# Optimization experiments

Measured on AMD Instinct MI355X. Metric: run time of the kernel, lower is better.

Reference implementation:

```python
import jax, jax.numpy as jnp
import numpy as np

ALPHA = 0.005
SCALE = 0.001
DELTA = 0.1
MAX_ITER = 50
EARLY = True


def setup_inputs() -> dict:
    key = jax.random.key(0)
    k1, k2, k3 = jax.random.split(key, 3)
    B, S, M, N = 32, 8, 512, 512
    x = jax.random.uniform(k1, (B, S, N), dtype=jnp.float32)
    A = jax.random.normal(k2, (B, S, M, N), dtype=jnp.float32) * 0.1
    b = jax.random.uniform(k3, (B, S, M), dtype=jnp.float32)
    return {"x": x, "A": A, "b": b}


def reference(x, A, b):
    # x: [B,S,N] primal iterate; A: [B,S,M,N] constraint matrices; b: [B,S,M]
    B, S = b.shape[0], b.shape[1]
    active0 = jnp.ones((B, S), dtype=bool)

    def body(carry, _):
        x_, active, stopped = carry
        # torch loop runs an iteration only while any(active) and not early-stopped
        run = jnp.any(active) & (~stopped)
        # Ax - b, clamped at 0 -> per-constraint violation
        Ax = jnp.einsum('bsn,bsmn->bsm', x_, A)          # [B,S,M]
        viol = jnp.clip(Ax - b, 0.0)
        new_active = jnp.sum(viol, axis=-1) >= DELTA      # ~(total < delta)
        stop_early = jnp.asarray(EARLY) & (~jnp.any(new_active))
        g = jnp.einsum('bsm,bsmn->bsn', viol, A)          # penalty gradient [B,S,N]
        lr = ALPHA / (1.0 + SCALE * g)
        x_upd = jnp.where(new_active[..., None], x_ - lr * g, x_)
        x_upd = jnp.clip(x_upd, 0.0)                      # clamp applied even to inactive rows
        # early stop happens BEFORE the update/clamp in the torch code
        x_new = jnp.where(stop_early, x_, x_upd)
        x_out = jnp.where(run, x_new, x_)
        active_out = jnp.where(run, new_active, active)
        stopped_out = stopped | (run & stop_early)
        return (x_out, active_out, stopped_out), None

    # torch: break when count > max_iter after increment -> up to max_iter+1 updates
    init = (x, active0, jnp.array(False))
    (x_final, _, _), _ = jax.lax.scan(body, init, None, length=MAX_ITER + 1)
    return x_final
```

## Files before the change

### kernel.cpp

```cpp
#include <hip/hip_runtime.h>

#define ALPHA 0.005f
#define SCALE 0.001f
#define DELTA 0.1f
#define MAXIT 51

constexpr int N = 512;
constexpr int M = 512;
constexpr int NTHREADS = 1024;
constexpr int NWAVES = NTHREADS / 64;
constexpr int MPW = M / NWAVES;
constexpr int NROWS = 256;
constexpr size_t WS_NEEDED = (size_t)NROWS * M * N * 2;

template<int CTRL>
__device__ __forceinline__ float dpp_mov(float v) {
    return __int_as_float(__builtin_amdgcn_update_dpp(
        0, __float_as_int(v), CTRL, 0xF, 0xF, true));
}

__device__ __forceinline__ float wave_sum_u(float d) {
    d += dpp_mov<0x111>(d);
    d += dpp_mov<0x112>(d);
    d += dpp_mov<0x114>(d);
    d += dpp_mov<0x118>(d);
    d += dpp_mov<0x142>(d);
    d += dpp_mov<0x143>(d);
    return __int_as_float(__builtin_amdgcn_readlane(__float_as_int(d), 63));
}

__device__ __forceinline__ float dot8(const float4& a, const float4& c,
                                      const float4& xa, const float4& xb) {
    return a.x*xa.x + a.y*xa.y + a.z*xa.z + a.w*xa.w
         + c.x*xb.x + c.y*xb.y + c.z*xb.z + c.w*xb.w;
}

__device__ __forceinline__ unsigned pack2_bf16(float f0, float f1) {
    unsigned a = __float_as_uint(f0); a += 0x7fffu + ((a >> 16) & 1u);
    unsigned b = __float_as_uint(f1); b += 0x7fffu + ((b >> 16) & 1u);
    return (a >> 16) | (b & 0xffff0000u);
}
__device__ __forceinline__ float bflo(unsigned u) { return __uint_as_float(u << 16); }
__device__ __forceinline__ float bfhi(unsigned u) { return __uint_as_float(u & 0xffff0000u); }

__global__ __launch_bounds__(NTHREADS, 4)
void lva_bf16_kernel(const float* __restrict__ x_in,
                     const float* __restrict__ A,
                     const float* __restrict__ bvec,
                     float* __restrict__ x_out,
                     unsigned short* __restrict__ wsA)
{
    __shared__ float b_lds[M];
    __shared__ float g_lds[NWAVES * N];
    __shared__ float sv_lds[NWAVES];
    __shared__ int bc_active;

    const int tid  = threadIdx.x;
    const int lane = tid & 63;
    const int w    = tid >> 6;
    const int r    = blockIdx.x;

    if (tid < M) b_lds[tid] = bvec[(size_t)r * M + tid];

    const int n0 = lane * 4;
    const int n1 = 256 + lane * 4;

    const float* xrow = x_in + (size_t)r * N;
    float4 xa = *(const float4*)(xrow + n0);
    float4 xb = *(const float4*)(xrow + n1);

    const float* Ablk = A + (size_t)r * M * N + (size_t)w * N;
    unsigned short* Wblk = wsA + (size_t)r * M * N + (size_t)w * N;

    __syncthreads();

    bool alive = true;

    {
        float4 ga = make_float4(0.f, 0.f, 0.f, 0.f);
        float4 gb = make_float4(0.f, 0.f, 0.f, 0.f);
        float sviol = 0.f;

        #pragma unroll 1
        for (int kk = 0; kk < MPW; kk += 4) {
            const float* p0 = Ablk + (size_t)(kk + 0) * (16 * N);
            const float* p1 = Ablk + (size_t)(kk + 1) * (16 * N);
            const float* p2 = Ablk + (size_t)(kk + 2) * (16 * N);
            const float* p3 = Ablk + (size_t)(kk + 3) * (16 * N);
            float4 a0 = *(const float4*)(p0 + n0), c0 = *(const float4*)(p0 + n1);
            float4 a1 = *(const float4*)(p1 + n0), c1 = *(const float4*)(p1 + n1);
            float4 a2 = *(const float4*)(p2 + n0), c2 = *(const float4*)(p2 + n1);
            float4 a3 = *(const float4*)(p3 + n0), c3 = *(const float4*)(p3 + n1);
            {
                unsigned short* q0 = Wblk + (size_t)(kk + 0) * (16 * N);
                unsigned short* q1 = Wblk + (size_t)(kk + 1) * (16 * N);
                unsigned short* q2 = Wblk + (size_t)(kk + 2) * (16 * N);
                unsigned short* q3 = Wblk + (size_t)(kk + 3) * (16 * N);
                *(uint2*)(q0 + n0) = make_uint2(pack2_bf16(a0.x, a0.y), pack2_bf16(a0.z, a0.w));
                *(uint2*)(q0 + n1) = make_uint2(pack2_bf16(c0.x, c0.y), pack2_bf16(c0.z, c0.w));
                *(uint2*)(q1 + n0) = make_uint2(pack2_bf16(a1.x, a1.y), pack2_bf16(a1.z, a1.w));
                *(uint2*)(q1 + n1) = make_uint2(pack2_bf16(c1.x, c1.y), pack2_bf16(c1.z, c1.w));
                *(uint2*)(q2 + n0) = make_uint2(pack2_bf16(a2.x, a2.y), pack2_bf16(a2.z, a2.w));
                *(uint2*)(q2 + n1) = make_uint2(pack2_bf16(c2.x, c2.y), pack2_bf16(c2.z, c2.w));
                *(uint2*)(q3 + n0) = make_uint2(pack2_bf16(a3.x, a3.y), pack2_bf16(a3.z, a3.w));
                *(uint2*)(q3 + n1) = make_uint2(pack2_bf16(c3.x, c3.y), pack2_bf16(c3.z, c3.w));
            }
            float bb0 = b_lds[w + 16 * (kk + 0)];
            float bb1 = b_lds[w + 16 * (kk + 1)];
            float bb2 = b_lds[w + 16 * (kk + 2)];
            float bb3 = b_lds[w + 16 * (kk + 3)];
            float d0 = wave_sum_u(dot8(a0, c0, xa, xb));
            float d1 = wave_sum_u(dot8(a1, c1, xa, xb));
            float d2 = wave_sum_u(dot8(a2, c2, xa, xb));
            float d3 = wave_sum_u(dot8(a3, c3, xa, xb));
            float v0 = fmaxf(d0 - bb0, 0.f);
            float v1 = fmaxf(d1 - bb1, 0.f);
            float v2 = fmaxf(d2 - bb2, 0.f);
            float v3 = fmaxf(d3 - bb3, 0.f);
            sviol += v0 + v1 + v2 + v3;
            ga.x += v0*a0.x + v1*a1.x + v2*a2.x + v3*a3.x;
            ga.y += v0*a0.y + v1*a1.y + v2*a2.y + v3*a3.y;
            ga.z += v0*a0.z + v1*a1.z + v2*a2.z + v3*a3.z;
            ga.w += v0*a0.w + v1*a1.w + v2*a2.w + v3*a3.w;
            gb.x += v0*c0.x + v1*c1.x + v2*c2.x + v3*c3.x;
            gb.y += v0*c0.y + v1*c1.y + v2*c2.y + v3*c3.y;
            gb.z += v0*c0.z + v1*c1.z + v2*c2.z + v3*c3.z;
            gb.w += v0*c0.w + v1*c1.w + v2*c2.w + v3*c3.w;
        }

        if (lane == 0) sv_lds[w] = sviol;
        *(float4*)(&g_lds[w * N + n0]) = ga;
        *(float4*)(&g_lds[w * N + n1]) = gb;
        __syncthreads();
        if (tid == 0) {
            float s = 0.f;
            #pragma unroll
            for (int i = 0; i < NWAVES; ++i) s += sv_lds[i];
            bc_active = (s >= DELTA) ? 1 : 0;
        }
        if (tid < N) {
            float s = 0.f;
            #pragma unroll
            for (int i = 0; i < NWAVES; ++i) s += g_lds[i * N + tid];
            g_lds[tid] = s;
        }
        __syncthreads();
        if (!bc_active) {
            alive = false;
        } else {
            float4 gfa = *(const float4*)(&g_lds[n0]);
            float4 gfb = *(const float4*)(&g_lds[n1]);
            xa.x = fmaxf(xa.x - (ALPHA / (1.f + SCALE*gfa.x)) * gfa.x, 0.f);
            xa.y = fmaxf(xa.y - (ALPHA / (1.f + SCALE*gfa.y)) * gfa.y, 0.f);
            xa.z = fmaxf(xa.z - (ALPHA / (1.f + SCALE*gfa.z)) * gfa.z, 0.f);
            xa.w = fmaxf(xa.w - (ALPHA / (1.f + SCALE*gfa.w)) * gfa.w, 0.f);
            xb.x = fmaxf(xb.x - (ALPHA / (1.f + SCALE*gfb.x)) * gfb.x, 0.f);
            xb.y = fmaxf(xb.y - (ALPHA / (1.f + SCALE*gfb.y)) * gfb.y, 0.f);
            xb.z = fmaxf(xb.z - (ALPHA / (1.f + SCALE*gfb.z)) * gfb.z, 0.f);
            xb.w = fmaxf(xb.w - (ALPHA / (1.f + SCALE*gfb.w)) * gfb.w, 0.f);
            __syncthreads();
        }
    }

    if (alive) {
        for (int t = 1; t < MAXIT; ++t) {
            float4 ga = make_float4(0.f, 0.f, 0.f, 0.f);
            float4 gb = make_float4(0.f, 0.f, 0.f, 0.f);
            float sviol = 0.f;

            #pragma unroll 1
            for (int kk = 0; kk < MPW; kk += 8) {
                uint2 qa[8], qb[8];
                #pragma unroll
                for (int j = 0; j < 8; ++j) {
                    const unsigned short* p = Wblk + (size_t)(kk + j) * (16 * N);
                    qa[j] = *(const uint2*)(p + n0);
                    qb[j] = *(const uint2*)(p + n1);
                }
                float d[8];
                #pragma unroll
                for (int j = 0; j < 8; ++j)
                    d[j] = bflo(qa[j].x)*xa.x + bfhi(qa[j].x)*xa.y
                         + bflo(qa[j].y)*xa.z + bfhi(qa[j].y)*xa.w
                         + bflo(qb[j].x)*xb.x + bfhi(qb[j].x)*xb.y
                         + bflo(qb[j].y)*xb.z + bfhi(qb[j].y)*xb.w;
                #pragma unroll
                for (int j = 0; j < 8; ++j) d[j] = wave_sum_u(d[j]);
                #pragma unroll
                for (int j = 0; j < 8; ++j) {
                    float v = fmaxf(d[j] - b_lds[w + 16 * (kk + j)], 0.f);
                    sviol += v;
                    ga.x += v*bflo(qa[j].x); ga.y += v*bfhi(qa[j].x);
                    ga.z += v*bflo(qa[j].y); ga.w += v*bfhi(qa[j].y);
                    gb.x += v*bflo(qb[j].x); gb.y += v*bfhi(qb[j].x);
                    gb.z += v*bflo(qb[j].y); gb.w += v*bfhi(qb[j].y);
                }
            }

            if (lane == 0) sv_lds[w] = sviol;
            *(float4*)(&g_lds[w * N + n0]) = ga;
            *(float4*)(&g_lds[w * N + n1]) = gb;
            __syncthreads();
            if (tid == 0) {
                float s = 0.f;
                #pragma unroll
                for (int i = 0; i < NWAVES; ++i) s += sv_lds[i];
                bc_active = (s >= DELTA) ? 1 : 0;
            }
            if (tid < N) {
                float s = 0.f;
                #pragma unroll
                for (int i = 0; i < NWAVES; ++i) s += g_lds[i * N + tid];
                g_lds[tid] = s;
            }
            __syncthreads();
            if (!bc_active) break;

            float4 gfa = *(const float4*)(&g_lds[n0]);
            float4 gfb = *(const float4*)(&g_lds[n1]);
            xa.x = fmaxf(xa.x - (ALPHA / (1.f + SCALE*gfa.x)) * gfa.x, 0.f);
            xa.y = fmaxf(xa.y - (ALPHA / (1.f + SCALE*gfa.y)) * gfa.y, 0.f);
            xa.z = fmaxf(xa.z - (ALPHA / (1.f + SCALE*gfa.z)) * gfa.z, 0.f);
            xa.w = fmaxf(xa.w - (ALPHA / (1.f + SCALE*gfa.w)) * gfa.w, 0.f);
            xb.x = fmaxf(xb.x - (ALPHA / (1.f + SCALE*gfb.x)) * gfb.x, 0.f);
            xb.y = fmaxf(xb.y - (ALPHA / (1.f + SCALE*gfb.y)) * gfb.y, 0.f);
            xb.z = fmaxf(xb.z - (ALPHA / (1.f + SCALE*gfb.z)) * gfb.z, 0.f);
            xb.w = fmaxf(xb.w - (ALPHA / (1.f + SCALE*gfb.w)) * gfb.w, 0.f);
            __syncthreads();
        }
    }

    float* orow = x_out + (size_t)r * N;
    if (w == 0) {
        *(float4*)(orow + n0) = xa;
        *(float4*)(orow + n1) = xb;
    }
}

__global__ __launch_bounds__(NTHREADS, 4)
void lva_kernel(const float* __restrict__ x_in,
                const float* __restrict__ A,
                const float* __restrict__ bvec,
                float* __restrict__ x_out)
{
    __shared__ float b_lds[M];
    __shared__ float g_lds[NWAVES * N];
    __shared__ float sv_lds[NWAVES];
    __shared__ int bc_active;

    const int tid  = threadIdx.x;
    const int lane = tid & 63;
    const int w    = tid >> 6;
    const int r    = blockIdx.x;

    if (tid < M) b_lds[tid] = bvec[(size_t)r * M + tid];

    const int n0 = lane * 4;
    const int n1 = 256 + lane * 4;

    const float* xrow = x_in + (size_t)r * N;
    float4 xa = *(const float4*)(xrow + n0);
    float4 xb = *(const float4*)(xrow + n1);

    const float* Ablk = A + (size_t)r * M * N + (size_t)w * N;

    __syncthreads();

    for (int t = 0; t < MAXIT; ++t) {
        float4 ga = make_float4(0.f, 0.f, 0.f, 0.f);
        float4 gb = make_float4(0.f, 0.f, 0.f, 0.f);
        float sviol = 0.f;

        #pragma unroll 1
        for (int kk = 0; kk < MPW; kk += 4) {
            const float* p0 = Ablk + (size_t)(kk + 0) * (16 * N);
            const float* p1 = Ablk + (size_t)(kk + 1) * (16 * N);
            const float* p2 = Ablk + (size_t)(kk + 2) * (16 * N);
            const float* p3 = Ablk + (size_t)(kk + 3) * (16 * N);
            float4 a0 = *(const float4*)(p0 + n0), c0 = *(const float4*)(p0 + n1);
            float4 a1 = *(const float4*)(p1 + n0), c1 = *(const float4*)(p1 + n1);
            float4 a2 = *(const float4*)(p2 + n0), c2 = *(const float4*)(p2 + n1);
            float4 a3 = *(const float4*)(p3 + n0), c3 = *(const float4*)(p3 + n1);
            float bb0 = b_lds[w + 16 * (kk + 0)];
            float bb1 = b_lds[w + 16 * (kk + 1)];
            float bb2 = b_lds[w + 16 * (kk + 2)];
            float bb3 = b_lds[w + 16 * (kk + 3)];
            float d0 = wave_sum_u(dot8(a0, c0, xa, xb));
            float d1 = wave_sum_u(dot8(a1, c1, xa, xb));
            float d2 = wave_sum_u(dot8(a2, c2, xa, xb));
            float d3 = wave_sum_u(dot8(a3, c3, xa, xb));
            float v0 = fmaxf(d0 - bb0, 0.f);
            float v1 = fmaxf(d1 - bb1, 0.f);
            float v2 = fmaxf(d2 - bb2, 0.f);
            float v3 = fmaxf(d3 - bb3, 0.f);
            sviol += v0 + v1 + v2 + v3;
            ga.x += v0*a0.x + v1*a1.x + v2*a2.x + v3*a3.x;
            ga.y += v0*a0.y + v1*a1.y + v2*a2.y + v3*a3.y;
            ga.z += v0*a0.z + v1*a1.z + v2*a2.z + v3*a3.z;
            ga.w += v0*a0.w + v1*a1.w + v2*a2.w + v3*a3.w;
            gb.x += v0*c0.x + v1*c1.x + v2*c2.x + v3*c3.x;
            gb.y += v0*c0.y + v1*c1.y + v2*c2.y + v3*c3.y;
            gb.z += v0*c0.z + v1*c1.z + v2*c2.z + v3*c3.z;
            gb.w += v0*c0.w + v1*c1.w + v2*c2.w + v3*c3.w;
        }

        if (lane == 0) sv_lds[w] = sviol;
        *(float4*)(&g_lds[w * N + n0]) = ga;
        *(float4*)(&g_lds[w * N + n1]) = gb;
        __syncthreads();
        if (tid == 0) {
            float s = 0.f;
            #pragma unroll
            for (int i = 0; i < NWAVES; ++i) s += sv_lds[i];
            bc_active = (s >= DELTA) ? 1 : 0;
        }
        if (tid < N) {
            float s = 0.f;
            #pragma unroll
            for (int i = 0; i < NWAVES; ++i) s += g_lds[i * N + tid];
            g_lds[tid] = s;
        }
        __syncthreads();
        if (!bc_active) break;

        float4 gfa = *(const float4*)(&g_lds[n0]);
        float4 gfb = *(const float4*)(&g_lds[n1]);
        xa.x = fmaxf(xa.x - (ALPHA / (1.f + SCALE*gfa.x)) * gfa.x, 0.f);
        xa.y = fmaxf(xa.y - (ALPHA / (1.f + SCALE*gfa.y)) * gfa.y, 0.f);
        xa.z = fmaxf(xa.z - (ALPHA / (1.f + SCALE*gfa.z)) * gfa.z, 0.f);
        xa.w = fmaxf(xa.w - (ALPHA / (1.f + SCALE*gfa.w)) * gfa.w, 0.f);
        xb.x = fmaxf(xb.x - (ALPHA / (1.f + SCALE*gfb.x)) * gfb.x, 0.f);
        xb.y = fmaxf(xb.y - (ALPHA / (1.f + SCALE*gfb.y)) * gfb.y, 0.f);
        xb.z = fmaxf(xb.z - (ALPHA / (1.f + SCALE*gfb.z)) * gfb.z, 0.f);
        xb.w = fmaxf(xb.w - (ALPHA / (1.f + SCALE*gfb.w)) * gfb.w, 0.f);
        __syncthreads();
    }

    float* orow = x_out + (size_t)r * N;
    if (w == 0) {
        *(float4*)(orow + n0) = xa;
        *(float4*)(orow + n1) = xb;
    }
}

extern "C" void kernel_launch(void* const* d_in, const int* in_sizes, int n_in,
                              void* d_out, int out_size, void* d_ws, size_t ws_size,
                              hipStream_t stream)
{
    const float* x  = (const float*)d_in[0];
    const float* A  = (const float*)d_in[1];
    const float* b  = (const float*)d_in[2];
    float* out      = (float*)d_out;

    if (ws_size >= WS_NEEDED) {
        lva_bf16_kernel<<<dim3(NROWS), dim3(NTHREADS), 0, stream>>>(
            x, A, b, out, (unsigned short*)d_ws);
    } else {
        lva_kernel<<<dim3(NROWS), dim3(NTHREADS), 0, stream>>>(x, A, b, out);
    }
}
```

Measured before the change: 1.300 ms.

## Split each wave into two half-wave rows and software-pipeline bf16 loads

```diff
diff --git a/kernel.cpp b/kernel.cpp
--- a/kernel.cpp
+++ b/kernel.cpp
@@ -43,6 +43,10 @@
 __device__ __forceinline__ float bflo(unsigned u) { return __uint_as_float(u << 16); }
 __device__ __forceinline__ float bfhi(unsigned u) { return __uint_as_float(u & 0xffff0000u); }
 
+__device__ __forceinline__ void unpack4(uint2 u, float4& f) {
+    f.x = bflo(u.x); f.y = bfhi(u.x); f.z = bflo(u.y); f.w = bfhi(u.y);
+}
+
 __global__ __launch_bounds__(NTHREADS, 4)
 void lva_bf16_kernel(const float* __restrict__ x_in,
                      const float* __restrict__ A,
@@ -51,8 +55,8 @@
                      unsigned short* __restrict__ wsA)
 {
     __shared__ float b_lds[M];
-    __shared__ float g_lds[NWAVES * N];
-    __shared__ float sv_lds[NWAVES];
+    __shared__ float g_lds[2 * NWAVES * N];
+    __shared__ float sv_lds[2 * NWAVES];
     __shared__ int bc_active;
 
     const int tid  = threadIdx.x;
@@ -158,82 +162,132 @@
             xb.y = fmaxf(xb.y - (ALPHA / (1.f + SCALE*gfb.y)) * gfb.y, 0.f);
             xb.z = fmaxf(xb.z - (ALPHA / (1.f + SCALE*gfb.z)) * gfb.z, 0.f);
             xb.w = fmaxf(xb.w - (ALPHA / (1.f + SCALE*gfb.w)) * gfb.w, 0.f);
-            __syncthreads();
-        }
-    }
+        }
+    }
+
+    const int h = lane >> 5;
+    const int s = lane & 31;
+    __syncthreads();
+    if (w == 0) {
+        *(float4*)(&g_lds[n0]) = xa;
+        *(float4*)(&g_lds[n1]) = xb;
+    }
+    __syncthreads();
+    float4 xf0 = *(const float4*)(&g_lds[  0 + s * 4]);
+    float4 xf1 = *(const float4*)(&g_lds[128 + s * 4]);
+    float4 xf2 = *(const float4*)(&g_lds[256 + s * 4]);
+    float4 xf3 = *(const float4*)(&g_lds[384 + s * 4]);
+    __syncthreads();
 
     if (alive) {
+        const uint2* Wp = (const uint2*)(wsA + (size_t)r * M * N)
+                          + (w + 16 * h) * 128 + s;
+        const int mb = w + 16 * h;
+
+        uint2 c0, c1, c2, c3, p0, p1, p2, p3;
+
+        #define LOADG(b0, b1, b2, b3, Gn) do {  \
+            b0 = Wp[(Gn) * 4096];               \
+            b1 = Wp[(Gn) * 4096 + 32];          \
+            b2 = Wp[(Gn) * 4096 + 64];          \
+            b3 = Wp[(Gn) * 4096 + 96];          \
+        } while (0)
+
+        #define COMPUTE(b0, b1, b2, b3, G) do {                               \
+            float4 f0, f1, f2, f3;                                            \
+            unpack4(b0, f0); unpack4(b1, f1);                                 \
+            unpack4(b2, f2); unpack4(b3, f3);                                 \
+            float d = f0.x*xf0.x + f0.y*xf0.y + f0.z*xf0.z + f0.w*xf0.w       \
+                    + f1.x*xf1.x + f1.y*xf1.y + f1.z*xf1.z + f1.w*xf1.w       \
+                    + f2.x*xf2.x + f2.y*xf2.y + f2.z*xf2.z + f2.w*xf2.w       \
+                    + f3.x*xf3.x + f3.y*xf3.y + f3.z*xf3.z + f3.w*xf3.w;      \
+            d += dpp_mov<0xB1>(d);            \
+            d += dpp_mov<0x4E>(d);            \
+            d += dpp_mov<0x141>(d);           \
+            d += dpp_mov<0x140>(d);           \
+            d += __int_as_float(__builtin_amdgcn_ds_swizzle(                  \
+                     __float_as_int(d), 0x401F));        \
+            float v = fmaxf(d - b_lds[mb + 32 * (G)], 0.f);                   \
+            sviol += v;                                                       \
+            g0.x += v*f0.x; g0.y += v*f0.y; g0.z += v*f0.z; g0.w += v*f0.w;   \
+            g1.x += v*f1.x; g1.y += v*f1.y; g1.z += v*f1.z; g1.w += v*f1.w;   \
+            g2.x += v*f2.x; g2.y += v*f2.y; g2.z += v*f2.z; g2.w += v*f2.w;   \
+            g3.x += v*f3.x; g3.y += v*f3.y; g3.z += v*f3.z; g3.w += v*f3.w;   \
+        } while (0)
+
+        LOADG(c0, c1, c2, c3, 0);
+
         for (int t = 1; t < MAXIT; ++t) {
-            float4 ga = make_float4(0.f, 0.f, 0.f, 0.f);
-            float4 gb = make_float4(0.f, 0.f, 0.f, 0.f);
+            float4 g0 = make_float4(0.f, 0.f, 0.f, 0.f);
+            float4 g1 = make_float4(0.f, 0.f, 0.f, 0.f);
+            float4 g2 = make_float4(0.f, 0.f, 0.f, 0.f);
+            float4 g3 = make_float4(0.f, 0.f, 0.f, 0.f);
             float sviol = 0.f;
 
             #pragma unroll 1
-            for (int kk = 0; kk < MPW; kk += 8) {
-                uint2 qa[8], qb[8];
-                #pragma unroll
-                for (int j = 0; j < 8; ++j) {
-                    const unsigned short* p = Wblk + (size_t)(kk + j) * (16 * N);
-                    qa[j] = *(const uint2*)(p + n0);
-                    qb[j] = *(const uint2*)(p + n1);
-                }
-                float d[8];
-                #pragma unroll
-                for (int j = 0; j < 8; ++j)
-                    d[j] = bflo(qa[j].x)*xa.x + bfhi(qa[j].x)*xa.y
-                         + bflo(qa[j].y)*xa.z + bfhi(qa[j].y)*xa.w
-                         + bflo(qb[j].x)*xb.x + bfhi(qb[j].x)*xb.y
-                         + bflo(qb[j].y)*xb.z + bfhi(qb[j].y)*xb.w;
-                #pragma unroll
-                for (int j = 0; j < 8; ++j) d[j] = wave_sum_u(d[j]);
-                #pragma unroll
-                for (int j = 0; j < 8; ++j) {
-                    float v = fmaxf(d[j] - b_lds[w + 16 * (kk + j)], 0.f);
-                    sviol += v;
-                    ga.x += v*bflo(qa[j].x); ga.y += v*bfhi(qa[j].x);
-                    ga.z += v*bflo(qa[j].y); ga.w += v*bfhi(qa[j].y);
-                    gb.x += v*bflo(qb[j].x); gb.y += v*bfhi(qb[j].x);
-                    gb.z += v*bflo(qb[j].y); gb.w += v*bfhi(qb[j].y);
-                }
+            for (int G = 0; G < 16; G += 2) {
+                LOADG(p0, p1, p2, p3, G + 1);
+                COMPUTE(c0, c1, c2, c3, G);
+                LOADG(c0, c1, c2, c3, (G + 2) & 15);
+                COMPUTE(p0, p1, p2, p3, G + 1);
             }
 
-            if (lane == 0) sv_lds[w] = sviol;
-            *(float4*)(&g_lds[w * N + n0]) = ga;
-            *(float4*)(&g_lds[w * N + n1]) = gb;
+            if (s == 0) sv_lds[2 * w + h] = sviol;
+            {
+                const int gbase = (2 * w + h) * N + s * 4;
+                *(float4*)(&g_lds[gbase +   0]) = g0;
+                *(float4*)(&g_lds[gbase + 128]) = g1;
+                *(float4*)(&g_lds[gbase + 256]) = g2;
+                *(float4*)(&g_lds[gbase + 384]) = g3;
+            }
             __syncthreads();
             if (tid == 0) {
-                float s = 0.f;
+                float sacc = 0.f;
                 #pragma unroll
-                for (int i = 0; i < NWAVES; ++i) s += sv_lds[i];
-                bc_active = (s >= DELTA) ? 1 : 0;
+                for (int i = 0; i < 2 * NWAVES; ++i) sacc += sv_lds[i];
+                bc_active = (sacc >= DELTA) ? 1 : 0;
             }
             if (tid < N) {
-                float s = 0.f;
+                float sacc = 0.f;
                 #pragma unroll
-                for (int i = 0; i < NWAVES; ++i) s += g_lds[i * N + tid];
-                g_lds[tid] = s;
+                for (int i = 0; i < 2 * NWAVES; ++i) sacc += g_lds[i * N + tid];
+                g_lds[tid] = sacc;
             }
             __syncthreads();
             if (!bc_active) break;
 
-            float4 gfa = *(const float4*)(&g_lds[n0]);
-            float4 gfb = *(const float4*)(&g_lds[n1]);
-            xa.x = fmaxf(xa.x - (ALPHA / (1.f + SCALE*gfa.x)) * gfa.x, 0.f);
-            xa.y = fmaxf(xa.y - (ALPHA / (1.f + SCALE*gfa.y)) * gfa.y, 0.f);
-            xa.z = fmaxf(xa.z - (ALPHA / (1.f + SCALE*gfa.z)) * gfa.z, 0.f);
-            xa.w = fmaxf(xa.w - (ALPHA / (1.f + SCALE*gfa.w)) * gfa.w, 0.f);
-            xb.x = fmaxf(xb.x - (ALPHA / (1.f + SCALE*gfb.x)) * gfb.x, 0.f);
-            xb.y = fmaxf(xb.y - (ALPHA / (1.f + SCALE*gfb.y)) * gfb.y, 0.f);
-            xb.z = fmaxf(xb.z - (ALPHA / (1.f + SCALE*gfb.z)) * gfb.z, 0.f);
-            xb.w = fmaxf(xb.w - (ALPHA / (1.f + SCALE*gfb.w)) * gfb.w, 0.f);
+            float4 q0 = *(const float4*)(&g_lds[  0 + s * 4]);
+            float4 q1 = *(const float4*)(&g_lds[128 + s * 4]);
+            float4 q2 = *(const float4*)(&g_lds[256 + s * 4]);
+            float4 q3 = *(const float4*)(&g_lds[384 + s * 4]);
+            xf0.x = fmaxf(xf0.x - (ALPHA / (1.f + SCALE*q0.x)) * q0.x, 0.f);
+            xf0.y = fmaxf(xf0.y - (ALPHA / (1.f + SCALE*q0.y)) * q0.y, 0.f);
+            xf0.z = fmaxf(xf0.z - (ALPHA / (1.f + SCALE*q0.z)) * q0.z, 0.f);
+            xf0.w = fmaxf(xf0.w - (ALPHA / (1.f + SCALE*q0.w)) * q0.w, 0.f);
+            xf1.x = fmaxf(xf1.x - (ALPHA / (1.f + SCALE*q1.x)) * q1.x, 0.f);
+            xf1.y = fmaxf(xf1.y - (ALPHA / (1.f + SCALE*q1.y)) * q1.y, 0.f);
+            xf1.z = fmaxf(xf1.z - (ALPHA / (1.f + SCALE*q1.z)) * q1.z, 0.f);
+            xf1.w = fmaxf(xf1.w - (ALPHA / (1.f + SCALE*q1.w)) * q1.w, 0.f);
+            xf2.x = fmaxf(xf2.x - (ALPHA / (1.f + SCALE*q2.x)) * q2.x, 0.f);
+            xf2.y = fmaxf(xf2.y - (ALPHA / (1.f + SCALE*q2.y)) * q2.y, 0.f);
+            xf2.z = fmaxf(xf2.z - (ALPHA / (1.f + SCALE*q2.z)) * q2.z, 0.f);
+            xf2.w = fmaxf(xf2.w - (ALPHA / (1.f + SCALE*q2.w)) * q2.w, 0.f);
+            xf3.x = fmaxf(xf3.x - (ALPHA / (1.f + SCALE*q3.x)) * q3.x, 0.f);
+            xf3.y = fmaxf(xf3.y - (ALPHA / (1.f + SCALE*q3.y)) * q3.y, 0.f);
+            xf3.z = fmaxf(xf3.z - (ALPHA / (1.f + SCALE*q3.z)) * q3.z, 0.f);
+            xf3.w = fmaxf(xf3.w - (ALPHA / (1.f + SCALE*q3.w)) * q3.w, 0.f);
             __syncthreads();
         }
-    }
-
-    float* orow = x_out + (size_t)r * N;
-    if (w == 0) {
-        *(float4*)(orow + n0) = xa;
-        *(float4*)(orow + n1) = xb;
+        #undef LOADG
+        #undef COMPUTE
+    }
+
+    if (w == 0 && h == 0) {
+        float* orow = x_out + (size_t)r * N + s * 4;
+        *(float4*)(orow +   0) = xf0;
+        *(float4*)(orow + 128) = xf1;
+        *(float4*)(orow + 256) = xf2;
+        *(float4*)(orow + 384) = xf3;
     }
 }
 
@@ -309,16 +363,16 @@
         *(float4*)(&g_lds[w * N + n1]) = gb;
         __syncthreads();
         if (tid == 0) {
-            float s = 0.f;
+            float sacc = 0.f;
             #pragma unroll
-            for (int i = 0; i < NWAVES; ++i) s += sv_lds[i];
-            bc_active = (s >= DELTA) ? 1 : 0;
+            for (int i = 0; i < NWAVES; ++i) sacc += sv_lds[i];
+            bc_active = (sacc >= DELTA) ? 1 : 0;
         }
         if (tid < N) {
-            float s = 0.f;
+            float sacc = 0.f;
             #pragma unroll
-            for (int i = 0; i < NWAVES; ++i) s += g_lds[i * N + tid];
-            g_lds[tid] = s;
+            for (int i = 0; i < NWAVES; ++i) sacc += g_lds[i * N + tid];
+            g_lds[tid] = sacc;
         }
         __syncthreads();
         if (!bc_active) break;
```

New measurement: 1.285 ms. Within noise of the previous version (-1.1%).
